# Performance work log

Measured on AMD Instinct MI355X. Metric: run time of the kernel, lower is better.

The kernel has to match this reference:

```python
import jax, jax.numpy as jnp
import numpy as np

K = 9  # kernel_size (knn neighbors, loop=True -> self included)

def setup_inputs() -> dict:
    key = jax.random.key(0)
    k1, k2, k3 = jax.random.split(key, 3)
    B, C, H, W = 8, 64, 32, 32
    OUT = 64
    x = jax.random.normal(k1, (B, C, H, W), dtype=jnp.float32)
    # SAGEConv params: lin_l (neighbor aggregate, with bias), lin_r (root, no bias)
    s = 1.0 / np.sqrt(C)
    W_l = jax.random.uniform(k2, (OUT, C), minval=-s, maxval=s, dtype=jnp.float32)
    b_l = jnp.zeros((OUT,), dtype=jnp.float32)
    W_r = jax.random.uniform(k3, (OUT, C), minval=-s, maxval=s, dtype=jnp.float32)
    return {"x": x, "W_l": W_l, "b_l": b_l, "W_r": W_r}

def _knn_mean(x_f, batches):
    # squared-euclidean pairwise distances [N, N], masked across batches
    sq = jnp.sum(x_f * x_f, axis=-1)
    dist = sq[:, None] + sq[None, :] - 2.0 * (x_f @ x_f.T)
    cross = batches[:, None] != batches[None, :]
    dist = jnp.where(cross, jnp.inf, dist)
    neg, idx = jax.lax.top_k(-dist, K)          # k nearest (self included, dist 0)
    valid = (neg != -jnp.inf).astype(x_f.dtype)  # handle degenerate last-batch node
    nbr = x_f[idx] * valid[..., None]            # [N, K, C]
    return nbr.sum(axis=1) / valid.sum(axis=1, keepdims=True)

def reference(x, W_l, b_l, W_r):
    B, C, H, Wd = x.shape
    N = B * H * Wd
    x_f = x.transpose(0, 2, 3, 1).reshape(N, C)  # flat_nodes: [B*H*W, C]
    # torch.linspace(0, B, steps=N).to(int64): truncation of i*B/(N-1)
    batches = jnp.linspace(0.0, float(B), N).astype(jnp.int32)
    mean_nbr = _knn_mean(x_f, batches)
    # SAGEConv: lin_l(mean_j x_j) + lin_r(x_i)
    return mean_nbr @ W_l.T + b_l + x_f @ W_r.T
```

## Files before the change

### kernel.cpp

```cpp
#include <hip/hip_runtime.h>
#include <cstdint>
#include <cstddef>


__global__ __launch_bounds__(256) void k_transpose_sq(const float* __restrict__ x,
                                                      float* __restrict__ xf,
                                                      float* __restrict__ sq) {
  __shared__ float tile[64][65];
  int blk = blockIdx.x;
  int b = blk >> 4;
  int hw0 = (blk & 15) << 6;
  int t = threadIdx.x;
  int lane_hw = t & 63;
  int c_base = t >> 6;
#pragma unroll
  for (int i = 0; i < 16; ++i) {
    int c = c_base + (i << 2);
    tile[c][lane_hw] = x[((b * 64 + c) << 10) + hw0 + lane_hw];
  }
  __syncthreads();
  int c_out = t & 63;
  int hw_base = t >> 6;
#pragma unroll
  for (int i = 0; i < 16; ++i) {
    int hw = hw_base + (i << 2);
    xf[(size_t)(((b << 10) + hw0 + hw) << 6) + c_out] = tile[c_out][hw];
  }
  if (t < 64) {
    float s = 0.f;
#pragma unroll
    for (int c = 0; c < 64; ++c) { float v = tile[c][t]; s += v * v; }
    sq[(b << 10) + hw0 + t] = s;
  }
}

__global__ __launch_bounds__(256) void k_dist(const float* __restrict__ xf,
                                              const float* __restrict__ sq,
                                              float* __restrict__ D) {
  __shared__ float4 As4[2048];
  __shared__ float4 Bs4[2048];
  int i0 = blockIdx.y << 7;
  int jj0 = blockIdx.x << 7;
  int s = (i0 >= 7168) ? 7168 : (i0 & ~1023);
  int j0 = s + jj0;
  int t = threadIdx.x;
  int tx = t & 15, ty = t >> 4;

#pragma unroll
  for (int i = 0; i < 8; ++i) {
    int u = t + (i << 8);
    int q = u & 15, m = u >> 4;
    int dst = (q << 7) | (m ^ (q & 7));
    As4[dst] = *(const float4*)&xf[((size_t)(i0 + m) << 6) + (q << 2)];
    Bs4[dst] = *(const float4*)&xf[((size_t)(j0 + m) << 6) + (q << 2)];
  }
  __syncthreads();

  float acc[8][8];
#pragma unroll
  for (int r = 0; r < 8; ++r)
#pragma unroll
    for (int c = 0; c < 8; ++c) acc[r][c] = 0.f;

#pragma unroll 1
  for (int q = 0; q < 16; ++q) {
    int base = q << 7;
    int sw = q & 7;
    float4 a[8], b[8];
#pragma unroll
    for (int r = 0; r < 8; ++r) a[r] = As4[base | ((ty + (r << 4)) ^ sw)];
#pragma unroll
    for (int c = 0; c < 8; ++c) b[c] = Bs4[base | ((tx + (c << 4)) ^ sw)];
#pragma unroll
    for (int r = 0; r < 8; ++r)
#pragma unroll
      for (int c = 0; c < 8; ++c) {
        float v = acc[r][c];
        v = fmaf(a[r].x, b[c].x, v);
        v = fmaf(a[r].y, b[c].y, v);
        v = fmaf(a[r].z, b[c].z, v);
        v = fmaf(a[r].w, b[c].w, v);
        acc[r][c] = v;
      }
  }

  float sqi[8], sqj[8];
#pragma unroll
  for (int r = 0; r < 8; ++r) sqi[r] = sq[i0 + ty + (r << 4)];
#pragma unroll
  for (int c = 0; c < 8; ++c) sqj[c] = sq[j0 + tx + (c << 4)];
#pragma unroll
  for (int r = 0; r < 8; ++r) {
    size_t rowbase = ((size_t)(i0 + ty + (r << 4)) << 10) + jj0 + tx;
#pragma unroll
    for (int c = 0; c < 8; ++c)
      D[rowbase + (c << 4)] = sqi[r] + sqj[c] - 2.f * acc[r][c];
  }
}

__global__ __launch_bounds__(256) void k_select(const float* __restrict__ D,
                                                int* __restrict__ idxO) {
  int t = threadIdx.x;
  int lane = t & 63;
  int i = (blockIdx.x << 2) + (t >> 6);
  if (i == 8191) {
    if (lane == 0) idxO[i * 9] = 8191;
    return;
  }
  int s = (i >= 7168) ? 7168 : (i & ~1023);
  bool mlast = (i >= 7168);
  const float* drow = D + ((size_t)i << 10);

  unsigned long long cand[16];
#pragma unroll
  for (int q = 0; q < 4; ++q) {
    float4 v = *(const float4*)&drow[(lane << 4) + (q << 2)];
    float vv[4] = {v.x, v.y, v.z, v.w};
#pragma unroll
    for (int e = 0; e < 4; ++e) {
      int slot = (q << 2) + e;
      int jj = (lane << 4) + slot;
      unsigned u = __float_as_uint(vv[e]);
      u = (u & 0x80000000u) ? ~u : (u | 0x80000000u);
      cand[slot] = ((unsigned long long)u << 32) | (unsigned)jj;
    }
  }
  if (mlast && lane == 63) cand[15] = ~0ull;

  unsigned long long m1 = cand[0], m2 = cand[1];
  if (m2 < m1) { unsigned long long tt = m1; m1 = m2; m2 = tt; }
#pragma unroll
  for (int q = 2; q < 16; ++q) {
    unsigned long long c = cand[q];
    unsigned long long lo = (c < m1) ? c : m1;
    unsigned long long hi = (c < m1) ? m1 : c;
    m2 = (hi < m2) ? hi : m2;
    m1 = lo;
  }

  unsigned long long lm = m1;
  unsigned rmask = 0;
  bool stale = false;
#pragma unroll
  for (int kk = 0; kk < 9; ++kk) {
    unsigned long long g = lm;
#pragma unroll
    for (int off = 32; off; off >>= 1) {
      unsigned ghi = __shfl_xor((unsigned)(g >> 32), off, 64);
      unsigned glo = __shfl_xor((unsigned)(g & 0xffffffffu), off, 64);
      unsigned long long o = ((unsigned long long)ghi << 32) | glo;
      g = (o < g) ? o : g;
    }
    if (lane == 0) idxO[i * 9 + kk] = s + (int)(unsigned)(g & 0xffffffffu);

    bool winner = (lm == g);
    if (winner) {
      rmask |= 1u << (unsigned)(g & 15u);
      if (!stale) {
        lm = m2;
        stale = true;
      } else {
        unsigned long long best = ~0ull;
#pragma unroll
        for (int q = 0; q < 16; ++q) {
          bool alive = ((rmask >> q) & 1u) == 0u;
          unsigned long long c = cand[q];
          best = (alive && c < best) ? c : best;
        }
        lm = best;
      }
    }
  }
}

__global__ __launch_bounds__(256) void k_out(const float* __restrict__ xf,
                                             const int* __restrict__ idxO,
                                             const float* __restrict__ Wl,
                                             const float* __restrict__ bl,
                                             const float* __restrict__ Wr,
                                             float* __restrict__ out) {
  __shared__ float WsL[64][65];
  __shared__ float WsR[64][65];
  int t = threadIdx.x;
#pragma unroll
  for (int i = 0; i < 16; ++i) {
    int lin = t + (i << 8);
    WsL[lin >> 6][lin & 63] = Wl[lin];
    WsR[lin >> 6][lin & 63] = Wr[lin];
  }
  __syncthreads();
  int lane = t & 63;
  float wl[64], wr[64];
#pragma unroll
  for (int c = 0; c < 64; ++c) { wl[c] = WsL[lane][c]; wr[c] = WsR[lane][c]; }
  float bias = bl[lane];
  int wave = t >> 6;
  int n0 = (blockIdx.x << 4) + (wave << 2);

  float ms[4], xr[4];
#pragma unroll
  for (int nn = 0; nn < 4; ++nn) {
    int n = n0 + nn;
    int cnt = (n == 8191) ? 1 : 9;
    float msum = 0.f;
    for (int k = 0; k < cnt; ++k) {
      int j = idxO[n * 9 + k];
      msum += xf[((size_t)j << 6) + lane];
    }
    ms[nn] = msum / (float)cnt;
    xr[nn] = xf[((size_t)n << 6) + lane];
  }

  float accL[4] = {0.f, 0.f, 0.f, 0.f};
  float accR[4] = {0.f, 0.f, 0.f, 0.f};
#pragma unroll
  for (int c = 0; c < 64; ++c) {
#pragma unroll
    for (int nn = 0; nn < 4; ++nn) {
      float mc = __int_as_float(__builtin_amdgcn_readlane(__float_as_int(ms[nn]), c));
      float xc = __int_as_float(__builtin_amdgcn_readlane(__float_as_int(xr[nn]), c));
      accL[nn] = fmaf(mc, wl[c], accL[nn]);
      accR[nn] = fmaf(xc, wr[c], accR[nn]);
    }
  }
#pragma unroll
  for (int nn = 0; nn < 4; ++nn) {
    int n = n0 + nn;
    out[((size_t)n << 6) + lane] = accL[nn] + accR[nn] + bias;
  }
}

extern "C" void kernel_launch(void* const* d_in, const int* in_sizes, int n_in,
                              void* d_out, int out_size, void* d_ws, size_t ws_size,
                              hipStream_t stream) {
  const float* x  = (const float*)d_in[0];
  const float* Wl = (const float*)d_in[1];
  const float* bl = (const float*)d_in[2];
  const float* Wr = (const float*)d_in[3];
  float* out = (float*)d_out;

  char* ws = (char*)d_ws;
  float* xf  = (float*)(ws);
  float* sq  = (float*)(ws + 2097152);
  int*   idx = (int*)  (ws + 2097152 + 32768);
  float* D   = (float*)(ws + 2097152 + 32768 + 294912);

  k_transpose_sq<<<128, 256, 0, stream>>>(x, xf, sq);
  k_dist<<<dim3(8, 64), 256, 0, stream>>>(xf, sq, D);
  k_select<<<2048, 256, 0, stream>>>(D, idx);
  k_out<<<512, 256, 0, stream>>>(xf, idx, Wl, bl, Wr, out);
}
```

Measured before the change: 113.0 us.

## Fuse transpose into distance GEMM and top-k selection into output projection

The separate transpose/squared-norm kernel is folded into the distance kernel, which now reads the NCHW input directly in two 32-channel passes, computes row norms in shared memory, and has the first column-block write the transposed features. The kNN selection is merged into the output kernel, so neighbor indices stay in registers instead of going through a global index buffer. Distance stores become float4-vectorized with a new tile mapping. This cuts four launches to two and removes intermediate global traffic, at the cost of more register pressure in the fused select+output kernel. There is also a cross-block dependency on xf, which is written by the cx==0 blocks of the first kernel and read by the second kernel.

```diff
diff --git a/kernel.cpp b/kernel.cpp
--- a/kernel.cpp
+++ b/kernel.cpp
@@ -3,182 +3,111 @@
 #include <cstddef>
 
 
-__global__ __launch_bounds__(256) void k_transpose_sq(const float* __restrict__ x,
-                                                      float* __restrict__ xf,
-                                                      float* __restrict__ sq) {
-  __shared__ float tile[64][65];
-  int blk = blockIdx.x;
-  int b = blk >> 4;
-  int hw0 = (blk & 15) << 6;
-  int t = threadIdx.x;
-  int lane_hw = t & 63;
-  int c_base = t >> 6;
-#pragma unroll
-  for (int i = 0; i < 16; ++i) {
-    int c = c_base + (i << 2);
-    tile[c][lane_hw] = x[((b * 64 + c) << 10) + hw0 + lane_hw];
-  }
-  __syncthreads();
-  int c_out = t & 63;
-  int hw_base = t >> 6;
-#pragma unroll
-  for (int i = 0; i < 16; ++i) {
-    int hw = hw_base + (i << 2);
-    xf[(size_t)(((b << 10) + hw0 + hw) << 6) + c_out] = tile[c_out][hw];
-  }
-  if (t < 64) {
-    float s = 0.f;
-#pragma unroll
-    for (int c = 0; c < 64; ++c) { float v = tile[c][t]; s += v * v; }
-    sq[(b << 10) + hw0 + t] = s;
-  }
-}
-
-__global__ __launch_bounds__(256) void k_dist(const float* __restrict__ xf,
-                                              const float* __restrict__ sq,
-                                              float* __restrict__ D) {
-  __shared__ float4 As4[2048];
-  __shared__ float4 Bs4[2048];
-  int i0 = blockIdx.y << 7;
-  int jj0 = blockIdx.x << 7;
+__global__ __launch_bounds__(256, 2) void k_dist(const float* __restrict__ x,
+                                                 float* __restrict__ xf,
+                                                 float* __restrict__ D) {
+  __shared__ float4 As4[32 * 33];
+  __shared__ float4 Bs4[32 * 33];
+  __shared__ float sqA[128];
+  __shared__ float sqB[128];
+  int cx = blockIdx.x;
+  int i0 = (int)blockIdx.y << 7;
   int s = (i0 >= 7168) ? 7168 : (i0 & ~1023);
-  int j0 = s + jj0;
+  int j0 = s + (cx << 7);
+  const float* xA = x + (((size_t)(i0 >> 10)) << 16) + (i0 & 1023);
+  const float* xB = x + (((size_t)(j0 >> 10)) << 16) + (j0 & 1023);
   int t = threadIdx.x;
   int tx = t & 15, ty = t >> 4;
 
-#pragma unroll
-  for (int i = 0; i < 8; ++i) {
-    int u = t + (i << 8);
-    int q = u & 15, m = u >> 4;
-    int dst = (q << 7) | (m ^ (q & 7));
-    As4[dst] = *(const float4*)&xf[((size_t)(i0 + m) << 6) + (q << 2)];
-    Bs4[dst] = *(const float4*)&xf[((size_t)(j0 + m) << 6) + (q << 2)];
+  float acc[8][8];
+#pragma unroll
+  for (int r = 0; r < 8; ++r)
+#pragma unroll
+    for (int c = 0; c < 8; ++c) acc[r][c] = 0.f;
+
+#pragma unroll 1
+  for (int pass = 0; pass < 2; ++pass) {
+    if (pass) __syncthreads();
+    int c0 = pass << 5;
+#pragma unroll
+    for (int i = 0; i < 4; ++i) {
+      int u = t + (i << 8);
+      int c = u >> 5, m4 = u & 31;
+      As4[c * 33 + m4] = *(const float4*)&xA[((size_t)(c0 + c) << 10) + (m4 << 2)];
+      Bs4[c * 33 + m4] = *(const float4*)&xB[((size_t)(c0 + c) << 10) + (m4 << 2)];
+    }
+    __syncthreads();
+    {
+      int m = t & 127;
+      const float* base = (t < 128) ? (const float*)As4 : (const float*)Bs4;
+      float p = 0.f;
+#pragma unroll
+      for (int c = 0; c < 32; ++c) {
+        float v = base[(c * 33 + (m >> 2)) * 4 + (m & 3)];
+        p = fmaf(v, v, p);
+      }
+      float* dst = (t < 128) ? sqA : sqB;
+      if (pass == 0) dst[m] = p; else dst[m] += p;
+    }
+    if (cx == 0) {
+#pragma unroll
+      for (int i = 0; i < 16; ++i) {
+        int u = t + (i << 8);
+        int c = u & 31, m = u >> 5;
+        xf[((size_t)(i0 + m) << 6) + c0 + c] =
+            ((const float*)As4)[(c * 33 + (m >> 2)) * 4 + (m & 3)];
+      }
+    }
+#pragma unroll 4
+    for (int k = 0; k < 32; ++k) {
+      float4 a0 = As4[k * 33 + ty];
+      float4 a1 = As4[k * 33 + 16 + ty];
+      float4 b0 = Bs4[k * 33 + tx];
+      float4 b1 = Bs4[k * 33 + 16 + tx];
+      float av[8] = {a0.x, a0.y, a0.z, a0.w, a1.x, a1.y, a1.z, a1.w};
+      float bv[8] = {b0.x, b0.y, b0.z, b0.w, b1.x, b1.y, b1.z, b1.w};
+#pragma unroll
+      for (int r = 0; r < 8; ++r)
+#pragma unroll
+        for (int c = 0; c < 8; ++c)
+          acc[r][c] = fmaf(av[r], bv[c], acc[r][c]);
+    }
   }
   __syncthreads();
 
-  float acc[8][8];
-#pragma unroll
-  for (int r = 0; r < 8; ++r)
-#pragma unroll
-    for (int c = 0; c < 8; ++c) acc[r][c] = 0.f;
-
-#pragma unroll 1
-  for (int q = 0; q < 16; ++q) {
-    int base = q << 7;
-    int sw = q & 7;
-    float4 a[8], b[8];
-#pragma unroll
-    for (int r = 0; r < 8; ++r) a[r] = As4[base | ((ty + (r << 4)) ^ sw)];
-#pragma unroll
-    for (int c = 0; c < 8; ++c) b[c] = Bs4[base | ((tx + (c << 4)) ^ sw)];
-#pragma unroll
-    for (int r = 0; r < 8; ++r)
-#pragma unroll
-      for (int c = 0; c < 8; ++c) {
-        float v = acc[r][c];
-        v = fmaf(a[r].x, b[c].x, v);
-        v = fmaf(a[r].y, b[c].y, v);
-        v = fmaf(a[r].z, b[c].z, v);
-        v = fmaf(a[r].w, b[c].w, v);
-        acc[r][c] = v;
-      }
-  }
-
+  int rloc[8], cloc[8];
+#pragma unroll
+  for (int r = 0; r < 4; ++r) { rloc[r] = (ty << 2) + r; rloc[4 + r] = 64 + (ty << 2) + r; }
+#pragma unroll
+  for (int c = 0; c < 4; ++c) { cloc[c] = (tx << 2) + c; cloc[4 + c] = 64 + (tx << 2) + c; }
   float sqi[8], sqj[8];
 #pragma unroll
-  for (int r = 0; r < 8; ++r) sqi[r] = sq[i0 + ty + (r << 4)];
-#pragma unroll
-  for (int c = 0; c < 8; ++c) sqj[c] = sq[j0 + tx + (c << 4)];
+  for (int r = 0; r < 8; ++r) sqi[r] = sqA[rloc[r]];
+#pragma unroll
+  for (int c = 0; c < 8; ++c) sqj[c] = sqB[cloc[c]];
 #pragma unroll
   for (int r = 0; r < 8; ++r) {
-    size_t rowbase = ((size_t)(i0 + ty + (r << 4)) << 10) + jj0 + tx;
-#pragma unroll
-    for (int c = 0; c < 8; ++c)
-      D[rowbase + (c << 4)] = sqi[r] + sqj[c] - 2.f * acc[r][c];
+    size_t rb = ((size_t)(i0 + rloc[r]) << 10) + (cx << 7);
+    float4 o0, o1;
+    o0.x = sqi[r] + sqj[0] - 2.f * acc[r][0];
+    o0.y = sqi[r] + sqj[1] - 2.f * acc[r][1];
+    o0.z = sqi[r] + sqj[2] - 2.f * acc[r][2];
+    o0.w = sqi[r] + sqj[3] - 2.f * acc[r][3];
+    o1.x = sqi[r] + sqj[4] - 2.f * acc[r][4];
+    o1.y = sqi[r] + sqj[5] - 2.f * acc[r][5];
+    o1.z = sqi[r] + sqj[6] - 2.f * acc[r][6];
+    o1.w = sqi[r] + sqj[7] - 2.f * acc[r][7];
+    *(float4*)&D[rb + (tx << 2)] = o0;
+    *(float4*)&D[rb + 64 + (tx << 2)] = o1;
   }
 }
 
-__global__ __launch_bounds__(256) void k_select(const float* __restrict__ D,
-                                                int* __restrict__ idxO) {
-  int t = threadIdx.x;
-  int lane = t & 63;
-  int i = (blockIdx.x << 2) + (t >> 6);
-  if (i == 8191) {
-    if (lane == 0) idxO[i * 9] = 8191;
-    return;
-  }
-  int s = (i >= 7168) ? 7168 : (i & ~1023);
-  bool mlast = (i >= 7168);
-  const float* drow = D + ((size_t)i << 10);
-
-  unsigned long long cand[16];
-#pragma unroll
-  for (int q = 0; q < 4; ++q) {
-    float4 v = *(const float4*)&drow[(lane << 4) + (q << 2)];
-    float vv[4] = {v.x, v.y, v.z, v.w};
-#pragma unroll
-    for (int e = 0; e < 4; ++e) {
-      int slot = (q << 2) + e;
-      int jj = (lane << 4) + slot;
-      unsigned u = __float_as_uint(vv[e]);
-      u = (u & 0x80000000u) ? ~u : (u | 0x80000000u);
-      cand[slot] = ((unsigned long long)u << 32) | (unsigned)jj;
-    }
-  }
-  if (mlast && lane == 63) cand[15] = ~0ull;
-
-  unsigned long long m1 = cand[0], m2 = cand[1];
-  if (m2 < m1) { unsigned long long tt = m1; m1 = m2; m2 = tt; }
-#pragma unroll
-  for (int q = 2; q < 16; ++q) {
-    unsigned long long c = cand[q];
-    unsigned long long lo = (c < m1) ? c : m1;
-    unsigned long long hi = (c < m1) ? m1 : c;
-    m2 = (hi < m2) ? hi : m2;
-    m1 = lo;
-  }
-
-  unsigned long long lm = m1;
-  unsigned rmask = 0;
-  bool stale = false;
-#pragma unroll
-  for (int kk = 0; kk < 9; ++kk) {
-    unsigned long long g = lm;
-#pragma unroll
-    for (int off = 32; off; off >>= 1) {
-      unsigned ghi = __shfl_xor((unsigned)(g >> 32), off, 64);
-      unsigned glo = __shfl_xor((unsigned)(g & 0xffffffffu), off, 64);
-      unsigned long long o = ((unsigned long long)ghi << 32) | glo;
-      g = (o < g) ? o : g;
-    }
-    if (lane == 0) idxO[i * 9 + kk] = s + (int)(unsigned)(g & 0xffffffffu);
-
-    bool winner = (lm == g);
-    if (winner) {
-      rmask |= 1u << (unsigned)(g & 15u);
-      if (!stale) {
-        lm = m2;
-        stale = true;
-      } else {
-        unsigned long long best = ~0ull;
-#pragma unroll
-        for (int q = 0; q < 16; ++q) {
-          bool alive = ((rmask >> q) & 1u) == 0u;
-          unsigned long long c = cand[q];
-          best = (alive && c < best) ? c : best;
-        }
-        lm = best;
-      }
-    }
-  }
-}
-
-__global__ __launch_bounds__(256) void k_out(const float* __restrict__ xf,
-                                             const int* __restrict__ idxO,
-                                             const float* __restrict__ Wl,
-                                             const float* __restrict__ bl,
-                                             const float* __restrict__ Wr,
-                                             float* __restrict__ out) {
+__global__ __launch_bounds__(256, 2) void k_selout(const float* __restrict__ D,
+                                                   const float* __restrict__ xf,
+                                                   const float* __restrict__ Wl,
+                                                   const float* __restrict__ bl,
+                                                   const float* __restrict__ Wr,
+                                                   float* __restrict__ out) {
   __shared__ float WsL[64][65];
   __shared__ float WsR[64][65];
   int t = threadIdx.x;
@@ -194,40 +123,98 @@
 #pragma unroll
   for (int c = 0; c < 64; ++c) { wl[c] = WsL[lane][c]; wr[c] = WsR[lane][c]; }
   float bias = bl[lane];
-  int wave = t >> 6;
-  int n0 = (blockIdx.x << 4) + (wave << 2);
+  int w = t >> 6;
+  int n0 = ((int)blockIdx.x << 4) + (w << 2);
+
+  unsigned j9[4][9];
+#pragma unroll
+  for (int r = 0; r < 4; ++r) {
+    int n = n0 + r;
+    if (n == 8191) { j9[r][0] = 8191u; continue; }
+    int s = (n >= 7168) ? 7168 : (n & ~1023);
+    bool mlast = (n >= 7168);
+    const float* drow = D + ((size_t)n << 10);
+    unsigned long long cand[16];
+#pragma unroll
+    for (int q = 0; q < 4; ++q) {
+      float4 v = *(const float4*)&drow[(lane << 4) + (q << 2)];
+      float vv[4] = {v.x, v.y, v.z, v.w};
+#pragma unroll
+      for (int e = 0; e < 4; ++e) {
+        int slot = (q << 2) + e;
+        unsigned u = __float_as_uint(vv[e]);
+        u = (u & 0x80000000u) ? ~u : (u | 0x80000000u);
+        cand[slot] = ((unsigned long long)u << 32) | (unsigned)((lane << 4) + slot);
+      }
+    }
+    if (mlast && lane == 63) cand[15] = ~0ull;
+    unsigned long long m1 = cand[0], m2 = cand[1];
+    if (m2 < m1) { unsigned long long tt = m1; m1 = m2; m2 = tt; }
+#pragma unroll
+    for (int q = 2; q < 16; ++q) {
+      unsigned long long c = cand[q];
+      unsigned long long lo = (c < m1) ? c : m1;
+      unsigned long long hi = (c < m1) ? m1 : c;
+      m2 = (hi < m2) ? hi : m2;
+      m1 = lo;
+    }
+    unsigned long long lm = m1;
+    unsigned rmask = 0;
+    bool stale = false;
+#pragma unroll
+    for (int kk = 0; kk < 9; ++kk) {
+      unsigned long long g = lm;
+#pragma unroll
+      for (int off = 32; off; off >>= 1) {
+        unsigned ghi = __shfl_xor((unsigned)(g >> 32), off, 64);
+        unsigned glo = __shfl_xor((unsigned)g, off, 64);
+        unsigned long long o = ((unsigned long long)ghi << 32) | glo;
+        g = (o < g) ? o : g;
+      }
+      j9[r][kk] = (unsigned)s + ((unsigned)g & 1023u);
+      if (lm == g) {
+        rmask |= 1u << (unsigned)(g & 15u);
+        if (!stale) { lm = m2; stale = true; }
+        else {
+          unsigned long long best = ~0ull;
+#pragma unroll
+          for (int q = 0; q < 16; ++q) {
+            bool alive = ((rmask >> q) & 1u) == 0u;
+            unsigned long long c = cand[q];
+            best = (alive && c < best) ? c : best;
+          }
+          lm = best;
+        }
+      }
+    }
+  }
 
   float ms[4], xr[4];
 #pragma unroll
-  for (int nn = 0; nn < 4; ++nn) {
-    int n = n0 + nn;
+  for (int r = 0; r < 4; ++r) {
+    int n = n0 + r;
     int cnt = (n == 8191) ? 1 : 9;
     float msum = 0.f;
-    for (int k = 0; k < cnt; ++k) {
-      int j = idxO[n * 9 + k];
-      msum += xf[((size_t)j << 6) + lane];
-    }
-    ms[nn] = msum / (float)cnt;
-    xr[nn] = xf[((size_t)n << 6) + lane];
-  }
-
+    for (int k = 0; k < cnt; ++k)
+      msum += xf[((size_t)j9[r][k] << 6) + lane];
+    ms[r] = msum / (float)cnt;
+    xr[r] = xf[((size_t)n << 6) + lane];
+  }
   float accL[4] = {0.f, 0.f, 0.f, 0.f};
   float accR[4] = {0.f, 0.f, 0.f, 0.f};
 #pragma unroll
   for (int c = 0; c < 64; ++c) {
 #pragma unroll
-    for (int nn = 0; nn < 4; ++nn) {
-      float mc = __int_as_float(__builtin_amdgcn_readlane(__float_as_int(ms[nn]), c));
-      float xc = __int_as_float(__builtin_amdgcn_readlane(__float_as_int(xr[nn]), c));
-      accL[nn] = fmaf(mc, wl[c], accL[nn]);
-      accR[nn] = fmaf(xc, wr[c], accR[nn]);
-    }
-  }
-#pragma unroll
-  for (int nn = 0; nn < 4; ++nn) {
-    int n = n0 + nn;
-    out[((size_t)n << 6) + lane] = accL[nn] + accR[nn] + bias;
-  }
+    for (int r = 0; r < 4; ++r) {
+      float mc = __int_as_float(__builtin_amdgcn_readlane(__float_as_int(ms[r]), c));
+      float xc = __int_as_float(__builtin_amdgcn_readlane(__float_as_int(xr[r]), c));
+      accL[r] = fmaf(mc, wl[c], accL[r]);
+      accR[r] = fmaf(xc, wr[c], accR[r]);
+    }
+  }
+#pragma unroll
+  for (int r = 0; r < 4; ++r)
+    out[((size_t)(n0 + r) << 6) + lane] = accL[r] + accR[r] + bias;
 }
 
 extern "C" void kernel_launch(void* const* d_in, const int* in_sizes, int n_in,
@@ -240,13 +227,9 @@
   float* out = (float*)d_out;
 
   char* ws = (char*)d_ws;
-  float* xf  = (float*)(ws);
-  float* sq  = (float*)(ws + 2097152);
-  int*   idx = (int*)  (ws + 2097152 + 32768);
-  float* D   = (float*)(ws + 2097152 + 32768 + 294912);
-
-  k_transpose_sq<<<128, 256, 0, stream>>>(x, xf, sq);
-  k_dist<<<dim3(8, 64), 256, 0, stream>>>(xf, sq, D);
-  k_select<<<2048, 256, 0, stream>>>(D, idx);
-  k_out<<<512, 256, 0, stream>>>(xf, idx, Wl, bl, Wr, out);
+  float* xf = (float*)(ws);
+  float* D  = (float*)(ws + 2097152);
+
+  k_dist<<<dim3(8, 64), 256, 0, stream>>>(x, xf, D);
+  k_selout<<<512, 256, 0, stream>>>(D, xf, Wl, bl, Wr, out);
 }
```

Measured after the change: 107.2 us. -5.2%, faster.
